# Kernel tuning notes

Hardware: AMD Instinct MI355X
Metric: run time of the kernel (lower is better)

The kernel has to match this reference:

```python
import jax, jax.numpy as jnp
import numpy as np

N_NODES = 100000

def setup_inputs() -> dict:
    key = jax.random.key(0)
    ks = jax.random.split(key, 9)
    d_in, d_out, e_dim, E = 64, 64, 16, 1600000
    x = jax.random.normal(ks[0], (N_NODES, d_in), dtype=jnp.float32)
    edge_index = jax.random.randint(ks[1], (2, E), 0, N_NODES, dtype=jnp.int64)
    edge_attr = jax.random.normal(ks[2], (E, e_dim), dtype=jnp.float32)
    s = 0.1
    W_edge = jax.random.normal(ks[3], (e_dim, d_in), dtype=jnp.float32) * s
    b_edge = jax.random.normal(ks[4], (d_in,), dtype=jnp.float32) * s
    W1 = jax.random.normal(ks[5], (d_in, d_out), dtype=jnp.float32) * s
    b1 = jax.random.normal(ks[6], (d_out,), dtype=jnp.float32) * s
    W2 = jax.random.normal(ks[7], (d_out, d_out), dtype=jnp.float32) * s
    b2 = jax.random.normal(ks[8], (d_out,), dtype=jnp.float32) * s
    return {"x": x, "edge_index": edge_index, "edge_attr": edge_attr,
            "W_edge": W_edge, "b_edge": b_edge, "W1": W1, "b1": b1,
            "W2": W2, "b2": b2}

def reference(x, edge_index, edge_attr, W_edge, b_edge, W1, b1, W2, b2):
    eps = 0.0
    src, dst = edge_index[0], edge_index[1]
    # project edge features to node dim (GINEConv lin with edge_dim set)
    e = edge_attr @ W_edge + b_edge                 # [E, d_in]
    msg = jax.nn.relu(x[src] + e)                   # gather + add + ReLU
    aggr = jax.ops.segment_sum(msg, dst, num_segments=N_NODES)  # scatter-sum
    h = (1.0 + eps) * x + aggr                      # [N, d_in]
    # 2-layer MLP update
    return jax.nn.relu(h @ W1 + b1) @ W2 + b2
```

## Files before the change

### kernel.cpp

```cpp
#include <hip/hip_runtime.h>

#define D 64
#define EDIM 16
#define CAP 64

#define T_A    2048
#define BSHIFT 9
#define BRANGE 512
#define BCAP   9216

__global__ __launch_bounds__(256) void coarse_bin_kernel(
    const int* __restrict__ dst, const int* __restrict__ src,
    long long* __restrict__ coarse, int* __restrict__ gcursor, int E)
{
    __shared__ long long      stage[T_A];
    __shared__ unsigned short stage_b[T_A];
    __shared__ int lcnt[256];
    __shared__ int loff[256];
    __shared__ int lbase[256];
    __shared__ int s_valid;

    const int t    = threadIdx.x;
    const int base = blockIdx.x * T_A;

    lcnt[t] = 0;
    __syncthreads();

    int       myb[8];
    int       myslot[8];
    long long myrec[8];
#pragma unroll
    for (int j = 0; j < 8; ++j) {
        const int i = base + t + j * 256;
        if (i < E) {
            const int d = dst[i];
            const int s = src[i];
            const int b = d >> BSHIFT;
            myb[j]   = b;
            myrec[j] = (long long)(unsigned)s
                     | ((long long)i << 17)
                     | ((long long)(d & (BRANGE - 1)) << 38);
            myslot[j] = atomicAdd(&lcnt[b], 1);
        } else {
            myb[j] = -1;
        }
    }
    __syncthreads();

    const int v = lcnt[t];
    loff[t] = v;
    __syncthreads();
    for (int off = 1; off < 256; off <<= 1) {
        const int add = (t >= off) ? loff[t - off] : 0;
        __syncthreads();
        loff[t] += add;
        __syncthreads();
    }
    if (t == 255) s_valid = loff[255];
    const int excl = loff[t] - v;
    loff[t] = excl;
    if (v > 0) lbase[t] = atomicAdd(&gcursor[t * 16], v);
    else       lbase[t] = 0;
    __syncthreads();

#pragma unroll
    for (int j = 0; j < 8; ++j) {
        if (myb[j] >= 0) {
            const int p = loff[myb[j]] + myslot[j];
            stage[p]   = myrec[j];
            stage_b[p] = (unsigned short)myb[j];
        }
    }
    __syncthreads();

    const int nv = s_valid;
    for (int p = t; p < nv; p += 256) {
        const int b   = stage_b[p];
        const int rel = lbase[b] + (p - loff[b]);
        if (rel < BCAP)
            coarse[(size_t)b * BCAP + rel] = stage[p];
    }
}

__global__ __launch_bounds__(1024) void refine_kernel(
    const long long* __restrict__ coarse, const int* __restrict__ gcursor,
    int2* __restrict__ rec, int* __restrict__ cnt, int N)
{
    __shared__ int lc[BRANGE];
    const int t = threadIdx.x;
    const int b = blockIdx.x;

    if (t < BRANGE) lc[t] = 0;
    __syncthreads();

    const int m = min(gcursor[b * 16], BCAP);
    const long long* crs = coarse + (size_t)b * BCAP;

    for (int i = t; i < m; i += 1024) {
        const long long p = crs[i];
        const int s    = (int)(p & 0x1FFFF);
        const int eid  = (int)((p >> 17) & 0x1FFFFF);
        const int dlo  = (int)((p >> 38) & (BRANGE - 1));
        const int slot = atomicAdd(&lc[dlo], 1);
        if (slot < CAP) {
            const int node = (b << BSHIFT) + dlo;
            rec[(size_t)node * CAP + slot] = make_int2(s, eid);
        }
    }
    __syncthreads();

    if (t < BRANGE) {
        const int node = (b << BSHIFT) + t;
        if (node < N) cnt[node] = min(lc[t], CAP);
    }
}

__global__ __launch_bounds__(256, 4) void gather_mlp_kernel(
    const float* __restrict__ x,
    const int2*  __restrict__ rec,
    const int*   __restrict__ cnt,
    const float* __restrict__ edge_attr,
    const float* __restrict__ W_edge,
    const float* __restrict__ b_edge,
    const float* __restrict__ W1, const float* __restrict__ b1,
    const float* __restrict__ W2, const float* __restrict__ b2,
    float*       __restrict__ out,
    int N)
{
    __shared__ float W1s[D * D];
    __shared__ float W2s[D * D];
    __shared__ float hstage[4][D];
    __shared__ float tstage[4][D];

    const int t = threadIdx.x;
    {
        const float4* w1v = (const float4*)W1;
        const float4* w2v = (const float4*)W2;
        float4* w1s = (float4*)W1s;
        float4* w2s = (float4*)W2s;
#pragma unroll
        for (int i = 0; i < 4; ++i) {
            w1s[t + i * 256] = w1v[t + i * 256];
            w2s[t + i * 256] = w2v[t + i * 256];
        }
    }
    __syncthreads();

    const int lane = t & 63;
    const int u    = lane >> 4;
    const int c    = lane & 15;
    const int wv   = t >> 6;
    const int wave   = blockIdx.x * 4 + wv;
    const int nwaves = gridDim.x * 4;

    float4 we[EDIM];
#pragma unroll
    for (int k = 0; k < EDIM; ++k)
        we[k] = *(const float4*)(W_edge + k * D + 4 * c);
    const float4 be  = *(const float4*)(b_edge + 4 * c);
    const float  b1v = b1[lane];
    const float  b2v = b2[lane];

    for (int n = wave; n < N; n += nwaves) {
        const int deg = min(cnt[n], CAP);
        const int2* bucket = rec + (size_t)n * CAP;
        float4 acc = make_float4(0.0f, 0.0f, 0.0f, 0.0f);

        for (int e = 0; e < deg; e += 4) {
            const int   ee  = e + u;
            const bool  ok  = ee < deg;
            const int   ec  = ok ? ee : (deg - 1);
            const float msk = ok ? 1.0f : 0.0f;

            const int2   r  = bucket[ec];
            const float4 xv = *(const float4*)(x + (size_t)r.x * D + 4 * c);

            const float4* ap = (const float4*)(edge_attr + (size_t)r.y * EDIM);
            const float4 a0 = ap[0], a1 = ap[1], a2 = ap[2], a3 = ap[3];
            const float av[EDIM] = {a0.x, a0.y, a0.z, a0.w,
                                    a1.x, a1.y, a1.z, a1.w,
                                    a2.x, a2.y, a2.z, a2.w,
                                    a3.x, a3.y, a3.z, a3.w};
            float4 v = be;
#pragma unroll
            for (int k = 0; k < EDIM; ++k) {
                v.x = fmaf(av[k], we[k].x, v.x);
                v.y = fmaf(av[k], we[k].y, v.y);
                v.z = fmaf(av[k], we[k].z, v.z);
                v.w = fmaf(av[k], we[k].w, v.w);
            }
            acc.x = fmaf(fmaxf(xv.x + v.x, 0.0f), msk, acc.x);
            acc.y = fmaf(fmaxf(xv.y + v.y, 0.0f), msk, acc.y);
            acc.z = fmaf(fmaxf(xv.z + v.z, 0.0f), msk, acc.z);
            acc.w = fmaf(fmaxf(xv.w + v.w, 0.0f), msk, acc.w);
        }

#pragma unroll
        for (int off = 16; off < 64; off <<= 1) {
            acc.x += __shfl_xor(acc.x, off, 64);
            acc.y += __shfl_xor(acc.y, off, 64);
            acc.z += __shfl_xor(acc.z, off, 64);
            acc.w += __shfl_xor(acc.w, off, 64);
        }

        if (u == 0) {
            const float4 xn = *(const float4*)(x + (size_t)n * D + 4 * c);
            float4 o;
            o.x = xn.x + acc.x;
            o.y = xn.y + acc.y;
            o.z = xn.z + acc.z;
            o.w = xn.w + acc.w;
            *(float4*)(&hstage[wv][4 * c]) = o;
        }
        asm volatile("s_waitcnt lgkmcnt(0)" ::: "memory");

        float acc1 = b1v;
#pragma unroll
        for (int k = 0; k < D; k += 4) {
            const float4 hv = *(const float4*)(&hstage[wv][k]);
            acc1 = fmaf(hv.x, W1s[(k + 0) * D + lane], acc1);
            acc1 = fmaf(hv.y, W1s[(k + 1) * D + lane], acc1);
            acc1 = fmaf(hv.z, W1s[(k + 2) * D + lane], acc1);
            acc1 = fmaf(hv.w, W1s[(k + 3) * D + lane], acc1);
        }
        tstage[wv][lane] = fmaxf(acc1, 0.0f);
        asm volatile("s_waitcnt lgkmcnt(0)" ::: "memory");

        float acc2 = b2v;
#pragma unroll
        for (int k = 0; k < D; k += 4) {
            const float4 tv = *(const float4*)(&tstage[wv][k]);
            acc2 = fmaf(tv.x, W2s[(k + 0) * D + lane], acc2);
            acc2 = fmaf(tv.y, W2s[(k + 1) * D + lane], acc2);
            acc2 = fmaf(tv.z, W2s[(k + 2) * D + lane], acc2);
            acc2 = fmaf(tv.w, W2s[(k + 3) * D + lane], acc2);
        }
        out[(size_t)n * D + lane] = acc2;
        asm volatile("s_waitcnt lgkmcnt(0)" ::: "memory");
    }
}

__global__ __launch_bounds__(256) void mlp_kernel(
    const float* __restrict__ W1, const float* __restrict__ b1,
    const float* __restrict__ W2, const float* __restrict__ b2,
    float* inout, int N)
{
    __shared__ float W1s[D * D];
    __shared__ float W2s[D * D];
    __shared__ float hbuf[4][D];
    __shared__ float tbuf[4][D];

    const int t = threadIdx.x;
    const float4* w1v = (const float4*)W1;
    const float4* w2v = (const float4*)W2;
    float4* w1s = (float4*)W1s;
    float4* w2s = (float4*)W2s;
#pragma unroll
    for (int i = 0; i < 4; ++i) {
        w1s[t + i * 256] = w1v[t + i * 256];
        w2s[t + i * 256] = w2v[t + i * 256];
    }
    __syncthreads();

    const int lane = t & 63;
    const int wv   = t >> 6;
    const float b1v = b1[lane];
    const float b2v = b2[lane];

    for (int base = blockIdx.x * 4; base < N; base += gridDim.x * 4) {
        const int    node = base + wv;
        const size_t off  = (size_t)node * D + lane;

        hbuf[wv][lane] = inout[off];
        __syncthreads();

        float acc = b1v;
#pragma unroll
        for (int k = 0; k < D; k += 4) {
            const float4 hv = *(const float4*)(&hbuf[wv][k]);
            acc = fmaf(hv.x, W1s[(k + 0) * D + lane], acc);
            acc = fmaf(hv.y, W1s[(k + 1) * D + lane], acc);
            acc = fmaf(hv.z, W1s[(k + 2) * D + lane], acc);
            acc = fmaf(hv.w, W1s[(k + 3) * D + lane], acc);
        }
        tbuf[wv][lane] = fmaxf(acc, 0.0f);
        __syncthreads();

        float acc2 = b2v;
#pragma unroll
        for (int k = 0; k < D; k += 4) {
            const float4 tv = *(const float4*)(&tbuf[wv][k]);
            acc2 = fmaf(tv.x, W2s[(k + 0) * D + lane], acc2);
            acc2 = fmaf(tv.y, W2s[(k + 1) * D + lane], acc2);
            acc2 = fmaf(tv.z, W2s[(k + 2) * D + lane], acc2);
            acc2 = fmaf(tv.w, W2s[(k + 3) * D + lane], acc2);
        }
        inout[off] = acc2;
        __syncthreads();
    }
}

__global__ __launch_bounds__(256) void edge_atomic_kernel(
    const float* __restrict__ x,
    const int*   __restrict__ src,
    const int*   __restrict__ dst,
    const float* __restrict__ edge_attr,
    const float* __restrict__ W_edge,
    const float* __restrict__ b_edge,
    float*       __restrict__ aggr,
    int E)
{
    const int lane   = threadIdx.x & 63;
    const int wave   = blockIdx.x * 4 + (threadIdx.x >> 6);
    const int nwaves = gridDim.x * 4;

    float we[EDIM];
#pragma unroll
    for (int k = 0; k < EDIM; ++k) we[k] = W_edge[k * D + lane];
    const float be = b_edge[lane];

    for (int i = wave; i < E; i += nwaves) {
        const int s = src[i];
        const int d = dst[i];
        const float4* eap = (const float4*)(edge_attr + (size_t)i * EDIM);
        float acc = be;
#pragma unroll
        for (int c = 0; c < 4; ++c) {
            const float4 ea = eap[c];
            acc = fmaf(ea.x, we[4 * c + 0], acc);
            acc = fmaf(ea.y, we[4 * c + 1], acc);
            acc = fmaf(ea.z, we[4 * c + 2], acc);
            acc = fmaf(ea.w, we[4 * c + 3], acc);
        }
        float m = fmaxf(x[(size_t)s * D + lane] + acc, 0.0f);
        atomicAdd(&aggr[(size_t)d * D + lane], m);
    }
}

__global__ __launch_bounds__(256) void add_x_kernel(
    const float* __restrict__ x, float* __restrict__ h, size_t n)
{
    size_t i = (size_t)blockIdx.x * blockDim.x + threadIdx.x;
    size_t stride = (size_t)gridDim.x * blockDim.x;
    for (; i < n; i += stride) h[i] += x[i];
}

extern "C" void kernel_launch(void* const* d_in, const int* in_sizes, int n_in,
                              void* d_out, int out_size, void* d_ws, size_t ws_size,
                              hipStream_t stream)
{
    const float* x      = (const float*)d_in[0];
    const int*   eidx   = (const int*)d_in[1];
    const float* eattr  = (const float*)d_in[2];
    const float* W_edge = (const float*)d_in[3];
    const float* b_edge = (const float*)d_in[4];
    const float* W1     = (const float*)d_in[5];
    const float* b1     = (const float*)d_in[6];
    const float* W2     = (const float*)d_in[7];
    const float* b2     = (const float*)d_in[8];
    float*       out    = (float*)d_out;

    const int E = in_sizes[1] / 2;
    const int N = in_sizes[0] / D;

    const int* src = eidx;
    const int* dst = eidx + E;

    const int kc = (N + BRANGE - 1) >> BSHIFT;

    const size_t sz_rec    = (size_t)N * CAP * sizeof(int2);
    const size_t sz_coarse = (size_t)kc * BCAP * sizeof(long long);
    const size_t sz_cnt    = (size_t)N * sizeof(int);
    const size_t sz_gcur   = 256 * 16 * sizeof(int);
    const size_t need      = sz_rec + sz_coarse + sz_cnt + sz_gcur;

    if (ws_size >= need) {
        char* p = (char*)d_ws;
        int2*      rec     = (int2*)p;                      p += sz_rec;
        long long* coarse  = (long long*)p;                 p += sz_coarse;
        int*       cnt     = (int*)p;                       p += sz_cnt;
        int*       gcursor = (int*)p;

        hipMemsetAsync(gcursor, 0, sz_gcur, stream);
        const int gridA = (E + T_A - 1) / T_A;
        coarse_bin_kernel<<<gridA, 256, 0, stream>>>(dst, src, coarse, gcursor, E);
        refine_kernel<<<kc, 1024, 0, stream>>>(coarse, gcursor, rec, cnt, N);
        gather_mlp_kernel<<<4096, 256, 0, stream>>>(x, rec, cnt,
                                                    eattr, W_edge, b_edge,
                                                    W1, b1, W2, b2, out, N);
    } else {
        hipMemsetAsync(out, 0, (size_t)N * D * sizeof(float), stream);
        edge_atomic_kernel<<<2048, 256, 0, stream>>>(x, src, dst, eattr,
                                                     W_edge, b_edge, out, E);
        add_x_kernel<<<1024, 256, 0, stream>>>(x, out, (size_t)N * D);
        mlp_kernel<<<2048, 256, 0, stream>>>(W1, b1, W2, b2, out, N);
    }
}
```

Measured before the change: 423.9 us.

## Sort refine bin records in shared memory before coalesced CSR writes

The refine kernel now counts per-node slots with shared atomics, prefix-scans the counts, and places each record into a dense shared-memory buffer of about 72KB grouped by destination node. It then writes the rec array with consecutive threads covering consecutive slots of each node, where before each record was scattered straight to global memory. This targets the uncoalesced global stores in the binning step. The cost is a large dynamic shared allocation that limits blocks per CU, a scan with many barriers, and extra shared-memory traffic.

```diff
diff --git a/kernel.cpp b/kernel.cpp
--- a/kernel.cpp
+++ b/kernel.cpp
@@ -82,11 +82,14 @@
     }
 }
 
-__global__ __launch_bounds__(1024) void refine_kernel(
+__global__ __launch_bounds__(1024) void refine_sort_kernel(
     const long long* __restrict__ coarse, const int* __restrict__ gcursor,
     int2* __restrict__ rec, int* __restrict__ cnt, int N)
 {
+    extern __shared__ long long dense[];
     __shared__ int lc[BRANGE];
+    __shared__ int bs[BRANGE];
+
     const int t = threadIdx.x;
     const int b = blockIdx.x;
 
@@ -96,21 +99,58 @@
     const int m = min(gcursor[b * 16], BCAP);
     const long long* crs = coarse + (size_t)b * BCAP;
 
-    for (int i = t; i < m; i += 1024) {
-        const long long p = crs[i];
-        const int s    = (int)(p & 0x1FFFF);
-        const int eid  = (int)((p >> 17) & 0x1FFFFF);
-        const int dlo  = (int)((p >> 38) & (BRANGE - 1));
-        const int slot = atomicAdd(&lc[dlo], 1);
-        if (slot < CAP) {
-            const int node = (b << BSHIFT) + dlo;
-            rec[(size_t)node * CAP + slot] = make_int2(s, eid);
-        }
-    }
-    __syncthreads();
-
+    long long rp[9];
+    int       rslot[9];
+    int       rdlo[9];
+    int       nmine = 0;
+#pragma unroll
+    for (int j = 0; j < 9; ++j) {
+        const int i = t + j * 1024;
+        if (i < m) {
+            const long long p = crs[i];
+            const int dlo = (int)((p >> 38) & (BRANGE - 1));
+            rp[j]    = p;
+            rdlo[j]  = dlo;
+            rslot[j] = atomicAdd(&lc[dlo], 1);
+            nmine    = j + 1;
+        }
+    }
+    __syncthreads();
+
+    if (t < BRANGE) bs[t] = lc[t];
+    __syncthreads();
+    for (int off = 1; off < BRANGE; off <<= 1) {
+        int add = 0;
+        if (t < BRANGE && t >= off) add = bs[t - off];
+        __syncthreads();
+        if (t < BRANGE) bs[t] += add;
+        __syncthreads();
+    }
+    if (t < BRANGE) bs[t] -= lc[t];
+    __syncthreads();
+
+#pragma unroll
+    for (int j = 0; j < 9; ++j) {
+        if (j < nmine)
+            dense[bs[rdlo[j]] + rslot[j]] = rp[j];
+    }
+    __syncthreads();
+
+    const int nodebase = b << BSHIFT;
+#pragma unroll
+    for (int j = 0; j < (BRANGE * CAP) / 1024; ++j) {
+        const int idx  = t + j * 1024;
+        const int r    = idx >> 6;
+        const int slot = idx & (CAP - 1);
+        const int c    = min(lc[r], CAP);
+        if (slot < c) {
+            const long long p = dense[bs[r] + slot];
+            rec[(size_t)(nodebase + r) * CAP + slot] =
+                make_int2((int)(p & 0x1FFFF), (int)((p >> 17) & 0x1FFFFF));
+        }
+    }
     if (t < BRANGE) {
-        const int node = (b << BSHIFT) + t;
+        const int node = nodebase + t;
         if (node < N) cnt[node] = min(lc[t], CAP);
     }
 }
@@ -384,7 +424,8 @@
         hipMemsetAsync(gcursor, 0, sz_gcur, stream);
         const int gridA = (E + T_A - 1) / T_A;
         coarse_bin_kernel<<<gridA, 256, 0, stream>>>(dst, src, coarse, gcursor, E);
-        refine_kernel<<<kc, 1024, 0, stream>>>(coarse, gcursor, rec, cnt, N);
+        refine_sort_kernel<<<kc, 1024, BCAP * sizeof(long long), stream>>>(
+            coarse, gcursor, rec, cnt, N);
         gather_mlp_kernel<<<4096, 256, 0, stream>>>(x, rec, cnt,
                                                     eattr, W_edge, b_edge,
                                                     W1, b1, W2, b2, out, N);
```

Result: no change. 425.3 us (+0.3%).
